# Performance work log

Hardware: AMD Instinct MI355X
Metric: run time of the kernel (lower is better)

Reference implementation:

```python
import jax, jax.numpy as jnp
import numpy as np

DIM = 512

def setup_inputs() -> dict:
    key = jax.random.key(0)
    kx, kq, kk, kv = jax.random.split(key, 4)
    x = jax.random.normal(kx, (8, 2048, DIM), dtype=jnp.float32)
    # Dense kernels are [in_dim, out_dim], no bias
    Wq = jax.random.normal(kq, (DIM, DIM), dtype=jnp.float32) * (DIM ** -0.5)
    Wk = jax.random.normal(kk, (DIM, DIM), dtype=jnp.float32) * (DIM ** -0.5)
    Wv = jax.random.normal(kv, (DIM, DIM), dtype=jnp.float32) * (DIM ** -0.5)
    return {"x": x, "Wq": Wq, "Wk": Wk, "Wv": Wv}

def reference(x, Wq, Wk, Wv):
    # x: [b, s, d]
    q = jnp.einsum('bsd,de->bse', x, Wq)
    k = jnp.einsum('bsd,de->bse', x, Wk)
    v = jnp.einsum('bsd,de->bse', x, Wv)
    scale = jnp.sqrt(jnp.asarray(DIM, dtype=x.dtype))
    attn = jnp.einsum('bqe,bke->bqk', q, k) / scale  # [b, s, s]
    attn = jax.nn.softmax(attn, axis=-1)
    return jnp.einsum('bqk,bke->bqe', attn, v)  # [b, s, d]
```

## Files before the change

kernel.cpp:

```cpp
#include <hip/hip_runtime.h>
#include <stdint.h>

typedef unsigned short u16;
typedef unsigned int u32;
typedef float floatx4 __attribute__((ext_vector_type(4)));
typedef __bf16 bf16x8 __attribute__((ext_vector_type(8)));
typedef __attribute__((address_space(1))) const u32 gu32;
typedef __attribute__((address_space(3))) u32 lu32;

#define SEQ 2048
#define DIM 512
#define NBATCH 8
#define TOTS (NBATCH * SEQ)

#if defined(__has_builtin)
#if __has_builtin(__builtin_amdgcn_cvt_pk_bf16_f32)
#define HAVE_PK_BF16 1
#endif
#endif
#ifndef HAVE_PK_BF16
#define HAVE_PK_BF16 0
#endif

__device__ __forceinline__ u16 f2bf(float f) {
#if HAVE_PK_BF16
  auto p = __builtin_amdgcn_cvt_pk_bf16_f32(f, f);
  union { decltype(p) v; u16 u[2]; } cv; cv.v = p;
  return cv.u[0];
#else
  u32 u = __float_as_uint(f);
  u += 0x7fffu + ((u >> 16) & 1u);
  return (u16)(u >> 16);
#endif
}


__device__ __forceinline__ void stageA(const u16* __restrict__ g, int ld, int k0, u16* lds) {
  const int t = threadIdx.x;
  const int wave = t >> 6, lane = t & 63;
  const int rsub = lane >> 3;
  const int lg = (lane & 7) ^ rsub;
#pragma unroll
  for (int q = 0; q < 4; ++q) {
    const int chunk = wave * 4 + q;
    const int row = chunk * 8 + rsub;
    const u16* gp = g + (size_t)row * ld + k0 + lg * 8;
    u16* lp = lds + chunk * 512 + lane * 8;
    __builtin_amdgcn_global_load_lds((gu32*)gp, (lu32*)lp, 16, 0, 0);
  }
}

__device__ __forceinline__ void stageB(const u16* __restrict__ g, int ld, int k0, u16* lds) {
  const int t = threadIdx.x;
  const int wave = t >> 6, lane = t & 63;
  const int rsub = lane >> 3;
  const int lg = (lane & 7) ^ rsub;
#pragma unroll
  for (int q = 0; q < 2; ++q) {
    const int chunk = wave * 2 + q;
    const int row = chunk * 8 + rsub;
    const u16* gp = g + (size_t)row * ld + k0 + lg * 8;
    u16* lp = lds + chunk * 512 + lane * 8;
    __builtin_amdgcn_global_load_lds((gu32*)gp, (lu32*)lp, 16, 0, 0);
  }
}

__device__ __forceinline__ void gemm_ring(const u16* __restrict__ A, int lda,
                                          const u16* __restrict__ BT, int ldb, int kdim,
                                          u16* As, u16* Bs, floatx4 acc[4][4]) {
  const int t = threadIdx.x;
  const int w = t >> 6, lane = t & 63;
  const int wm = w & 3, wn = w >> 2;
  const int l15 = lane & 15, quad = lane >> 4;
  const int swz = l15 & 7;
  const int nsteps = kdim >> 6;

  stageA(A, lda, 0, As);           stageB(BT, ldb, 0, Bs);
  stageA(A, lda, 64, As + 16384);  stageB(BT, ldb, 64, Bs + 8192);

  int slot = 0;
  for (int kt = 0; kt < nsteps; ++kt) {
    if (kt + 1 < nsteps) asm volatile("s_waitcnt vmcnt(6)" ::: "memory");
    else                 asm volatile("s_waitcnt vmcnt(0)" ::: "memory");
    __builtin_amdgcn_s_barrier();
    asm volatile("" ::: "memory");
    if (kt + 2 < nsteps) {
      int ss = slot + 2; if (ss >= 3) ss -= 3;
      stageA(A, lda, (kt + 2) << 6, As + ss * 16384);
      stageB(BT, ldb, (kt + 2) << 6, Bs + ss * 8192);
    }
    const u16* Ac = As + slot * 16384;
    const u16* Bc = Bs + slot * 8192;
#pragma unroll
    for (int ks = 0; ks < 2; ++ks) {
      const int pg = ((ks << 2) + quad) ^ swz;
      bf16x8 af[4], bfr[4];
#pragma unroll
      for (int i = 0; i < 4; ++i) {
        af[i]  = *(const bf16x8*)(Ac + (wm * 64 + i * 16 + l15) * 64 + pg * 8);
        bfr[i] = *(const bf16x8*)(Bc + (wn * 64 + i * 16 + l15) * 64 + pg * 8);
      }
#pragma unroll
      for (int mi = 0; mi < 4; ++mi)
#pragma unroll
        for (int ni = 0; ni < 4; ++ni)
          acc[mi][ni] = __builtin_amdgcn_mfma_f32_16x16x32_bf16(af[mi], bfr[ni], acc[mi][ni], 0, 0, 0);
    }
    ++slot; if (slot == 3) slot = 0;
  }
}

__device__ __forceinline__ void zero_acc(floatx4 acc[4][4]) {
#pragma unroll
  for (int i = 0; i < 4; ++i)
#pragma unroll
    for (int j = 0; j < 4; ++j)
      acc[i][j] = (floatx4){0.f, 0.f, 0.f, 0.f};
}

__global__ __launch_bounds__(256) void k_prep(const float* __restrict__ x,
                                              const float* __restrict__ Wq, const float* __restrict__ Wk,
                                              const float* __restrict__ Wv,
                                              u16* __restrict__ xb, u16* __restrict__ wt) {
  __shared__ float tile[64][65];
  const int t = threadIdx.x;
  if (blockIdx.x < 4096) {
    size_t i = ((size_t)blockIdx.x * 256 + t) * 8;
    float4 a = *(const float4*)(x + i);
    float4 b = *(const float4*)(x + i + 4);
    u16 o[8] = {f2bf(a.x), f2bf(a.y), f2bf(a.z), f2bf(a.w),
                f2bf(b.x), f2bf(b.y), f2bf(b.z), f2bf(b.w)};
    *(uint4*)(xb + i) = *(const uint4*)o;
    return;
  }
  const int r = blockIdx.x - 4096;
  const int sec = r >> 6, rem = r & 63;
  const int kb = (rem & 7) * 64, nb0 = (rem >> 3) * 64;
  const float* W = (sec == 0) ? Wq : (sec == 1) ? Wk : Wv;
#pragma unroll
  for (int i = 0; i < 4; ++i) {
    int kr = i * 16 + (t >> 4), nc = (t & 15) * 4;
    float4 v = *(const float4*)&W[(size_t)(kb + kr) * 512 + nb0 + nc];
    tile[kr][nc] = v.x; tile[kr][nc + 1] = v.y; tile[kr][nc + 2] = v.z; tile[kr][nc + 3] = v.w;
  }
  __syncthreads();
#pragma unroll
  for (int i = 0; i < 4; ++i) {
    int nr = i * 16 + (t >> 4), kc = (t & 15) * 4;
    u16 o[4] = {f2bf(tile[kc][nr]), f2bf(tile[kc + 1][nr]), f2bf(tile[kc + 2][nr]), f2bf(tile[kc + 3][nr])};
    *(uint2*)&wt[(size_t)(sec * 512 + nb0 + nr) * 512 + kb + kc] = *(const uint2*)o;
  }
}

__global__ __launch_bounds__(512, 2) void k_proj(const u16* __restrict__ xb, const u16* __restrict__ wt,
                                                 u16* __restrict__ qo, u16* __restrict__ ko,
                                                 u16* __restrict__ vt) {
  __shared__ __align__(16) u16 As[3 * 256 * 64];
  __shared__ __align__(16) u16 Bs[3 * 128 * 64];
  const int gx = blockIdx.x;
  floatx4 acc[4][4];
  zero_acc(acc);
  const int t = threadIdx.x, w = t >> 6, lane = t & 63;
  const int wm = w & 3, wn = w >> 2;
  const int l15 = lane & 15, quad = lane >> 4;
  if (gx < 512) {
    const int m0 = (gx & 63) * 256, n0 = (gx >> 6) * 128;
    gemm_ring(xb + (size_t)m0 * DIM, DIM, wt + (size_t)n0 * DIM, DIM, DIM, As, Bs, acc);
    const int sec = n0 >> 9;
    u16* __restrict__ C = sec ? ko : qo;
    const float scl = sec ? 1.0f : 0.04419417382415922f;
#pragma unroll
    for (int mi = 0; mi < 4; ++mi)
#pragma unroll
      for (int ni = 0; ni < 4; ++ni)
#pragma unroll
        for (int r = 0; r < 4; ++r) {
          int m = m0 + wm * 64 + mi * 16 + quad * 4 + r;
          int nc = (n0 + wn * 64 + ni * 16 + l15) & 511;
          C[(size_t)m * DIM + nc] = f2bf(acc[mi][ni][r] * scl);
        }
  } else {
    const int rr = gx - 512;
    const int m0 = (rr & 1) * 256;
    const int n0 = (rr >> 1) * 128;
    gemm_ring(wt + (size_t)(2 * DIM + m0) * DIM, DIM, xb + (size_t)n0 * DIM, DIM, DIM, As, Bs, acc);
#pragma unroll
    for (int mi = 0; mi < 4; ++mi)
#pragma unroll
      for (int ni = 0; ni < 4; ++ni)
#pragma unroll
        for (int r = 0; r < 4; ++r) {
          int m = m0 + wm * 64 + mi * 16 + quad * 4 + r;
          int n = n0 + wn * 64 + ni * 16 + l15;
          vt[(size_t)m * TOTS + n] = f2bf(acc[mi][ni][r]);
        }
  }
}

__global__ __launch_bounds__(512, 2) void k_scores(const u16* __restrict__ q, const u16* __restrict__ kk,
                                                   u16* __restrict__ sc, float* __restrict__ rowsum,
                                                   int b0) {
  __shared__ __align__(16) u16 As[3 * 256 * 64];
  __shared__ __align__(16) u16 Bs[3 * 128 * 64];
  const int bz = blockIdx.z, bb = b0 + bz;
  const int xcd = blockIdx.x & 7, j = blockIdx.x >> 3;
  const int n0 = (xcd * 2 + (j & 1)) * 128;
  const int m0 = (j >> 1) * 256;
  floatx4 acc[4][4];
  zero_acc(acc);
  gemm_ring(q + (size_t)bb * SEQ * DIM + (size_t)m0 * DIM, DIM,
            kk + (size_t)bb * SEQ * DIM + (size_t)n0 * DIM, DIM, DIM, As, Bs, acc);
  u16* C = sc + (size_t)bz * SEQ * SEQ;
  float* rsb = rowsum + (size_t)bb * SEQ;
  const int t = threadIdx.x, w = t >> 6, lane = t & 63;
  const int wm = w & 3, wn = w >> 2;
  const int l15 = lane & 15, quad = lane >> 4;
#pragma unroll
  for (int mi = 0; mi < 4; ++mi)
#pragma unroll
    for (int r = 0; r < 4; ++r) {
      int m = m0 + wm * 64 + mi * 16 + quad * 4 + r;
      float p = 0.f;
      float ev[4];
#pragma unroll
      for (int ni = 0; ni < 4; ++ni) {
        ev[ni] = __expf(acc[mi][ni][r]);
        p += ev[ni];
      }
#pragma unroll
      for (int ni = 0; ni < 4; ++ni) {
        int n = n0 + wn * 64 + ni * 16 + l15;
        C[(size_t)m * SEQ + n] = f2bf(ev[ni]);
      }
      p += __shfl_xor(p, 1); p += __shfl_xor(p, 2);
      p += __shfl_xor(p, 4); p += __shfl_xor(p, 8);
      if (l15 == 0) atomicAdd(&rsb[m], p);
    }
}

__global__ __launch_bounds__(512, 2) void k_pv(const u16* __restrict__ sc, const u16* __restrict__ vt,
                                               const float* __restrict__ rowsum,
                                               float* __restrict__ out, int b0) {
  __shared__ __align__(16) u16 As[3 * 256 * 64];
  __shared__ __align__(16) u16 Bs[3 * 128 * 64];
  const int bz = blockIdx.z, bb = b0 + bz;
  const int xcd = blockIdx.x & 7, j = blockIdx.x >> 3;
  const int m0 = xcd * 256, n0 = j * 128;
  floatx4 acc[4][4];
  zero_acc(acc);
  gemm_ring(sc + (size_t)bz * SEQ * SEQ + (size_t)m0 * SEQ, SEQ,
            vt + (size_t)n0 * TOTS + (size_t)bb * SEQ, TOTS, SEQ, As, Bs, acc);
  float* C = out + (size_t)bb * SEQ * DIM;
  const float* rsb = rowsum + (size_t)bb * SEQ;
  const int t = threadIdx.x, w = t >> 6, lane = t & 63;
  const int wm = w & 3, wn = w >> 2;
  const int l15 = lane & 15, quad = lane >> 4;
#pragma unroll
  for (int mi = 0; mi < 4; ++mi)
#pragma unroll
    for (int r = 0; r < 4; ++r) {
      int m = m0 + wm * 64 + mi * 16 + quad * 4 + r;
      float inv = 1.0f / rsb[m];
#pragma unroll
      for (int ni = 0; ni < 4; ++ni) {
        int n = n0 + wn * 64 + ni * 16 + l15;
        C[(size_t)m * DIM + n] = acc[mi][ni][r] * inv;
      }
    }
}

extern "C" void kernel_launch(void* const* d_in, const int* in_sizes, int n_in,
                              void* d_out, int out_size, void* d_ws, size_t ws_size,
                              hipStream_t stream) {
  const float* x  = (const float*)d_in[0];
  const float* Wq = (const float*)d_in[1];
  const float* Wk = (const float*)d_in[2];
  const float* Wv = (const float*)d_in[3];
  float* out = (float*)d_out;
  char* ws = (char*)d_ws;

  u16* xb   = (u16*)(ws + 0);
  u16* wt   = (u16*)(ws + 16777216);
  u16* qo   = (u16*)(ws + 18350080);
  u16* ko   = (u16*)(ws + 35127296);
  u16* vt   = (u16*)(ws + 51904512);
  float* rs = (float*)(ws + 68681728);
  u16* sc   = (u16*)(ws + 68747264);
  const size_t base_need = 68747264;
  const size_t per_b = (size_t)SEQ * SEQ * 2;
  size_t avail = (ws_size > base_need) ? (ws_size - base_need) : 0;
  int nb = (int)(avail / per_b);
  if (nb < 1) nb = 1;
  if (nb > NBATCH) nb = NBATCH;

  hipMemsetAsync(rs, 0, (size_t)NBATCH * SEQ * sizeof(float), stream);
  k_prep<<<dim3(4288), dim3(256), 0, stream>>>(x, Wq, Wk, Wv, xb, wt);
  k_proj<<<dim3(768), dim3(512), 0, stream>>>(xb, wt, qo, ko, vt);
  for (int b0 = 0; b0 < NBATCH; b0 += nb) {
    int nbr = (NBATCH - b0 < nb) ? (NBATCH - b0) : nb;
    k_scores<<<dim3(128, 1, nbr), dim3(512), 0, stream>>>(qo, ko, sc, rs, b0);
    k_pv<<<dim3(32, 1, nbr), dim3(512), 0, stream>>>(sc, vt, rs, out, b0);
  }
}
```

Baseline: 234.1 us.

## Interleave global-to-LDS prefetch with MFMA sub-steps using ping-pong barriers and setprio

```diff
diff --git a/kernel.cpp b/kernel.cpp
--- a/kernel.cpp
+++ b/kernel.cpp
@@ -34,14 +34,21 @@
 #endif
 }
 
-
-__device__ __forceinline__ void stageA(const u16* __restrict__ g, int ld, int k0, u16* lds) {
+__device__ __forceinline__ void barrier_f() {
+  asm volatile("" ::: "memory");
+  __builtin_amdgcn_s_barrier();
+  asm volatile("" ::: "memory");
+}
+
+
+template<int PART>
+__device__ __forceinline__ void stageA_h(const u16* __restrict__ g, int ld, int k0, u16* lds) {
   const int t = threadIdx.x;
   const int wave = t >> 6, lane = t & 63;
   const int rsub = lane >> 3;
   const int lg = (lane & 7) ^ rsub;
 #pragma unroll
-  for (int q = 0; q < 4; ++q) {
+  for (int q = PART * 2; q < PART * 2 + 2; ++q) {
     const int chunk = wave * 4 + q;
     const int row = chunk * 8 + rsub;
     const u16* gp = g + (size_t)row * ld + k0 + lg * 8;
@@ -50,19 +57,24 @@
   }
 }
 
-__device__ __forceinline__ void stageB(const u16* __restrict__ g, int ld, int k0, u16* lds) {
+template<int PART>
+__device__ __forceinline__ void stageB_h(const u16* __restrict__ g, int ld, int k0, u16* lds) {
   const int t = threadIdx.x;
   const int wave = t >> 6, lane = t & 63;
   const int rsub = lane >> 3;
   const int lg = (lane & 7) ^ rsub;
-#pragma unroll
-  for (int q = 0; q < 2; ++q) {
-    const int chunk = wave * 2 + q;
-    const int row = chunk * 8 + rsub;
-    const u16* gp = g + (size_t)row * ld + k0 + lg * 8;
-    u16* lp = lds + chunk * 512 + lane * 8;
-    __builtin_amdgcn_global_load_lds((gu32*)gp, (lu32*)lp, 16, 0, 0);
-  }
+  const int chunk = wave * 2 + PART;
+  const int row = chunk * 8 + rsub;
+  const u16* gp = g + (size_t)row * ld + k0 + lg * 8;
+  u16* lp = lds + chunk * 512 + lane * 8;
+  __builtin_amdgcn_global_load_lds((gu32*)gp, (lu32*)lp, 16, 0, 0);
+}
+
+__device__ __forceinline__ void stageA(const u16* __restrict__ g, int ld, int k0, u16* lds) {
+  stageA_h<0>(g, ld, k0, lds); stageA_h<1>(g, ld, k0, lds);
+}
+__device__ __forceinline__ void stageB(const u16* __restrict__ g, int ld, int k0, u16* lds) {
+  stageB_h<0>(g, ld, k0, lds); stageB_h<1>(g, ld, k0, lds);
 }
 
 __device__ __forceinline__ void gemm_ring(const u16* __restrict__ A, int lda,
@@ -77,20 +89,16 @@
 
   stageA(A, lda, 0, As);           stageB(BT, ldb, 0, Bs);
   stageA(A, lda, 64, As + 16384);  stageB(BT, ldb, 64, Bs + 8192);
+  asm volatile("s_waitcnt vmcnt(6)" ::: "memory");
+  barrier_f();
 
   int slot = 0;
   for (int kt = 0; kt < nsteps; ++kt) {
-    if (kt + 1 < nsteps) asm volatile("s_waitcnt vmcnt(6)" ::: "memory");
-    else                 asm volatile("s_waitcnt vmcnt(0)" ::: "memory");
-    __builtin_amdgcn_s_barrier();
-    asm volatile("" ::: "memory");
-    if (kt + 2 < nsteps) {
-      int ss = slot + 2; if (ss >= 3) ss -= 3;
-      stageA(A, lda, (kt + 2) << 6, As + ss * 16384);
-      stageB(BT, ldb, (kt + 2) << 6, Bs + ss * 8192);
-    }
     const u16* Ac = As + slot * 16384;
     const u16* Bc = Bs + slot * 8192;
+    int ss = slot + 2; if (ss >= 3) ss -= 3;
+    const bool st = (kt + 2 < nsteps);
+    const int k2 = (kt + 2) << 6;
 #pragma unroll
     for (int ks = 0; ks < 2; ++ks) {
       const int pg = ((ks << 2) + quad) ^ swz;
@@ -100,11 +108,26 @@
         af[i]  = *(const bf16x8*)(Ac + (wm * 64 + i * 16 + l15) * 64 + pg * 8);
         bfr[i] = *(const bf16x8*)(Bc + (wn * 64 + i * 16 + l15) * 64 + pg * 8);
       }
+      if (st) {
+        if (ks == 0) { stageA_h<0>(A, lda, k2, As + ss * 16384); stageB_h<0>(BT, ldb, k2, Bs + ss * 8192); }
+        else         { stageA_h<1>(A, lda, k2, As + ss * 16384); stageB_h<1>(BT, ldb, k2, Bs + ss * 8192); }
+      }
+      barrier_f();
+      asm volatile("s_waitcnt lgkmcnt(0)" ::: "memory");
+      __builtin_amdgcn_sched_barrier(0);
+      __builtin_amdgcn_s_setprio(1);
 #pragma unroll
       for (int mi = 0; mi < 4; ++mi)
 #pragma unroll
         for (int ni = 0; ni < 4; ++ni)
           acc[mi][ni] = __builtin_amdgcn_mfma_f32_16x16x32_bf16(af[mi], bfr[ni], acc[mi][ni], 0, 0, 0);
+      __builtin_amdgcn_s_setprio(0);
+      __builtin_amdgcn_sched_barrier(0);
+      if (ks == 1) {
+        if (kt + 2 < nsteps)      asm volatile("s_waitcnt vmcnt(6)" ::: "memory");
+        else if (kt + 1 < nsteps) asm volatile("s_waitcnt vmcnt(0)" ::: "memory");
+      }
+      barrier_f();
     }
     ++slot; if (slot == 3) slot = 0;
   }
```

Measured after the change: 224.1 us. 1.04x faster.

## Enlarge GEMM tiles to 256x256 with double-buffered LDS and fold rowsum zeroing

Applied to the files above, without the earlier changes.

```diff
diff --git a/kernel.cpp b/kernel.cpp
--- a/kernel.cpp
+++ b/kernel.cpp
@@ -34,15 +34,22 @@
 #endif
 }
 
-
-__device__ __forceinline__ void stageA(const u16* __restrict__ g, int ld, int k0, u16* lds) {
+__device__ __forceinline__ void barrier_f() {
+  asm volatile("" ::: "memory");
+  __builtin_amdgcn_s_barrier();
+  asm volatile("" ::: "memory");
+}
+
+
+template<int NL>
+__device__ __forceinline__ void stage_t(const u16* __restrict__ g, int ld, int k0, u16* lds) {
   const int t = threadIdx.x;
   const int wave = t >> 6, lane = t & 63;
   const int rsub = lane >> 3;
   const int lg = (lane & 7) ^ rsub;
 #pragma unroll
-  for (int q = 0; q < 4; ++q) {
-    const int chunk = wave * 4 + q;
+  for (int q = 0; q < NL; ++q) {
+    const int chunk = wave * NL + q;
     const int row = chunk * 8 + rsub;
     const u16* gp = g + (size_t)row * ld + k0 + lg * 8;
     u16* lp = lds + chunk * 512 + lane * 8;
@@ -50,69 +57,67 @@
   }
 }
 
-__device__ __forceinline__ void stageB(const u16* __restrict__ g, int ld, int k0, u16* lds) {
-  const int t = threadIdx.x;
-  const int wave = t >> 6, lane = t & 63;
-  const int rsub = lane >> 3;
-  const int lg = (lane & 7) ^ rsub;
-#pragma unroll
-  for (int q = 0; q < 2; ++q) {
-    const int chunk = wave * 2 + q;
-    const int row = chunk * 8 + rsub;
-    const u16* gp = g + (size_t)row * ld + k0 + lg * 8;
-    u16* lp = lds + chunk * 512 + lane * 8;
-    __builtin_amdgcn_global_load_lds((gu32*)gp, (lu32*)lp, 16, 0, 0);
-  }
-}
-
-__device__ __forceinline__ void gemm_ring(const u16* __restrict__ A, int lda,
-                                          const u16* __restrict__ BT, int ldb, int kdim,
-                                          u16* As, u16* Bs, floatx4 acc[4][4]) {
+template<int MREP>
+__device__ __forceinline__ void gemm_big(const u16* __restrict__ A, int lda,
+                                         const u16* __restrict__ BT, int ldb, int kdim,
+                                         u16* As, u16* Bs, floatx4 acc[][4]) {
+  constexpr int ASLOT = MREP * 128 * 64;
+  constexpr int BSLOT = 256 * 64;
   const int t = threadIdx.x;
   const int w = t >> 6, lane = t & 63;
-  const int wm = w & 3, wn = w >> 2;
+  const int wm = w >> 2, wn = w & 3;
   const int l15 = lane & 15, quad = lane >> 4;
   const int swz = l15 & 7;
   const int nsteps = kdim >> 6;
 
-  stageA(A, lda, 0, As);           stageB(BT, ldb, 0, Bs);
-  stageA(A, lda, 64, As + 16384);  stageB(BT, ldb, 64, Bs + 8192);
-
-  int slot = 0;
+  stage_t<2 * MREP>(A, lda, 0, As);
+  stage_t<4>(BT, ldb, 0, Bs);
+
   for (int kt = 0; kt < nsteps; ++kt) {
-    if (kt + 1 < nsteps) asm volatile("s_waitcnt vmcnt(6)" ::: "memory");
-    else                 asm volatile("s_waitcnt vmcnt(0)" ::: "memory");
-    __builtin_amdgcn_s_barrier();
-    asm volatile("" ::: "memory");
-    if (kt + 2 < nsteps) {
-      int ss = slot + 2; if (ss >= 3) ss -= 3;
-      stageA(A, lda, (kt + 2) << 6, As + ss * 16384);
-      stageB(BT, ldb, (kt + 2) << 6, Bs + ss * 8192);
+    const u16* Ac = As + (kt & 1) * ASLOT;
+    const u16* Bc = Bs + (kt & 1) * BSLOT;
+    if (kt + 1 < nsteps) {
+      stage_t<2 * MREP>(A, lda, (kt + 1) << 6, As + ((kt + 1) & 1) * ASLOT);
+      stage_t<4>(BT, ldb, (kt + 1) << 6, Bs + ((kt + 1) & 1) * BSLOT);
+      if constexpr (MREP == 2) asm volatile("s_waitcnt vmcnt(8)" ::: "memory");
+      else                     asm volatile("s_waitcnt vmcnt(6)" ::: "memory");
+    } else {
+      asm volatile("s_waitcnt vmcnt(0)" ::: "memory");
     }
-    const u16* Ac = As + slot * 16384;
-    const u16* Bc = Bs + slot * 8192;
-#pragma unroll
-    for (int ks = 0; ks < 2; ++ks) {
-      const int pg = ((ks << 2) + quad) ^ swz;
-      bf16x8 af[4], bfr[4];
-#pragma unroll
-      for (int i = 0; i < 4; ++i) {
-        af[i]  = *(const bf16x8*)(Ac + (wm * 64 + i * 16 + l15) * 64 + pg * 8);
-        bfr[i] = *(const bf16x8*)(Bc + (wn * 64 + i * 16 + l15) * 64 + pg * 8);
-      }
+    barrier_f();
+
+    bf16x8 bfr[4];
+#pragma unroll
+    for (int p = 0; p < 2 * MREP; ++p) {
+      const int ksl = (MREP == 2) ? (p >> 1) : p;
+      const int mh  = (MREP == 2) ? (p & 1) : 0;
+      const int pg = ((ksl << 2) + quad) ^ swz;
+      if (mh == 0) {
+#pragma unroll
+        for (int i = 0; i < 4; ++i)
+          bfr[i] = *(const bf16x8*)(Bc + (wn * 64 + i * 16 + l15) * 64 + pg * 8);
+      }
+      bf16x8 af[4];
+#pragma unroll
+      for (int i = 0; i < 4; ++i)
+        af[i] = *(const bf16x8*)(Ac + (wm * MREP * 64 + mh * 64 + i * 16 + l15) * 64 + pg * 8);
+      __builtin_amdgcn_s_setprio(1);
 #pragma unroll
       for (int mi = 0; mi < 4; ++mi)
 #pragma unroll
         for (int ni = 0; ni < 4; ++ni)
-          acc[mi][ni] = __builtin_amdgcn_mfma_f32_16x16x32_bf16(af[mi], bfr[ni], acc[mi][ni], 0, 0, 0);
+          acc[mh * 4 + mi][ni] =
+              __builtin_amdgcn_mfma_f32_16x16x32_bf16(af[mi], bfr[ni], acc[mh * 4 + mi][ni], 0, 0, 0);
+      __builtin_amdgcn_s_setprio(0);
     }
-    ++slot; if (slot == 3) slot = 0;
-  }
-}
-
-__device__ __forceinline__ void zero_acc(floatx4 acc[4][4]) {
-#pragma unroll
-  for (int i = 0; i < 4; ++i)
+    barrier_f();
+  }
+}
+
+template<int NACC>
+__device__ __forceinline__ void zero_acc(floatx4 acc[][4]) {
+#pragma unroll
+  for (int i = 0; i < NACC; ++i)
 #pragma unroll
     for (int j = 0; j < 4; ++j)
       acc[i][j] = (floatx4){0.f, 0.f, 0.f, 0.f};
@@ -154,77 +159,82 @@
 
 __global__ __launch_bounds__(512, 2) void k_proj(const u16* __restrict__ xb, const u16* __restrict__ wt,
                                                  u16* __restrict__ qo, u16* __restrict__ ko,
-                                                 u16* __restrict__ vt) {
-  __shared__ __align__(16) u16 As[3 * 256 * 64];
-  __shared__ __align__(16) u16 Bs[3 * 128 * 64];
+                                                 u16* __restrict__ vt, float* __restrict__ rs) {
+  __shared__ __align__(16) u16 As[2 * 256 * 64];
+  __shared__ __align__(16) u16 Bs[2 * 256 * 64];
   const int gx = blockIdx.x;
-  floatx4 acc[4][4];
-  zero_acc(acc);
+  if (gx < 16) {
+    float4 z = {0.f, 0.f, 0.f, 0.f};
+    float* p = rs + ((size_t)gx * 512 + threadIdx.x) * 8;
+    *(float4*)p = z; *(float4*)(p + 4) = z;
+  }
+  floatx4 acc[8][4];
+  zero_acc<8>(acc);
   const int t = threadIdx.x, w = t >> 6, lane = t & 63;
-  const int wm = w & 3, wn = w >> 2;
+  const int wm = w >> 2, wn = w & 3;
   const int l15 = lane & 15, quad = lane >> 4;
-  if (gx < 512) {
-    const int m0 = (gx & 63) * 256, n0 = (gx >> 6) * 128;
-    gemm_ring(xb + (size_t)m0 * DIM, DIM, wt + (size_t)n0 * DIM, DIM, DIM, As, Bs, acc);
+  if (gx < 256) {
+    const int m0 = (gx & 63) * 256, n0 = (gx >> 6) * 256;
+    gemm_big<2>(xb + (size_t)m0 * DIM, DIM, wt + (size_t)n0 * DIM, DIM, DIM, As, Bs, acc);
     const int sec = n0 >> 9;
     u16* __restrict__ C = sec ? ko : qo;
     const float scl = sec ? 1.0f : 0.04419417382415922f;
 #pragma unroll
-    for (int mi = 0; mi < 4; ++mi)
-#pragma unroll
-      for (int ni = 0; ni < 4; ++ni)
-#pragma unroll
-        for (int r = 0; r < 4; ++r) {
-          int m = m0 + wm * 64 + mi * 16 + quad * 4 + r;
+    for (int a = 0; a < 8; ++a)
+#pragma unroll
+      for (int r = 0; r < 4; ++r) {
+        int m = m0 + wm * 128 + (a >> 2) * 64 + (a & 3) * 16 + quad * 4 + r;
+#pragma unroll
+        for (int ni = 0; ni < 4; ++ni) {
           int nc = (n0 + wn * 64 + ni * 16 + l15) & 511;
-          C[(size_t)m * DIM + nc] = f2bf(acc[mi][ni][r] * scl);
+          C[(size_t)m * DIM + nc] = f2bf(acc[a][ni][r] * scl);
         }
+      }
   } else {
-    const int rr = gx - 512;
+    const int rr = gx - 256;
     const int m0 = (rr & 1) * 256;
-    const int n0 = (rr >> 1) * 128;
-    gemm_ring(wt + (size_t)(2 * DIM + m0) * DIM, DIM, xb + (size_t)n0 * DIM, DIM, DIM, As, Bs, acc);
-#pragma unroll
-    for (int mi = 0; mi < 4; ++mi)
-#pragma unroll
-      for (int ni = 0; ni < 4; ++ni)
-#pragma unroll
-        for (int r = 0; r < 4; ++r) {
-          int m = m0 + wm * 64 + mi * 16 + quad * 4 + r;
+    const int n0 = (rr >> 1) * 256;
+    gemm_big<2>(wt + (size_t)(2 * DIM + m0) * DIM, DIM, xb + (size_t)n0 * DIM, DIM, DIM, As, Bs, acc);
+#pragma unroll
+    for (int a = 0; a < 8; ++a)
+#pragma unroll
+      for (int r = 0; r < 4; ++r) {
+        int m = m0 + wm * 128 + (a >> 2) * 64 + (a & 3) * 16 + quad * 4 + r;
+#pragma unroll
+        for (int ni = 0; ni < 4; ++ni) {
           int n = n0 + wn * 64 + ni * 16 + l15;
-          vt[(size_t)m * TOTS + n] = f2bf(acc[mi][ni][r]);
+          vt[(size_t)m * TOTS + n] = f2bf(acc[a][ni][r]);
         }
+      }
   }
 }
 
 __global__ __launch_bounds__(512, 2) void k_scores(const u16* __restrict__ q, const u16* __restrict__ kk,
                                                    u16* __restrict__ sc, float* __restrict__ rowsum,
                                                    int b0) {
-  __shared__ __align__(16) u16 As[3 * 256 * 64];
-  __shared__ __align__(16) u16 Bs[3 * 128 * 64];
+  __shared__ __align__(16) u16 As[2 * 256 * 64];
+  __shared__ __align__(16) u16 Bs[2 * 256 * 64];
   const int bz = blockIdx.z, bb = b0 + bz;
-  const int xcd = blockIdx.x & 7, j = blockIdx.x >> 3;
-  const int n0 = (xcd * 2 + (j & 1)) * 128;
-  const int m0 = (j >> 1) * 256;
-  floatx4 acc[4][4];
-  zero_acc(acc);
-  gemm_ring(q + (size_t)bb * SEQ * DIM + (size_t)m0 * DIM, DIM,
-            kk + (size_t)bb * SEQ * DIM + (size_t)n0 * DIM, DIM, DIM, As, Bs, acc);
+  const int m0 = (blockIdx.x >> 3) * 256, n0 = (blockIdx.x & 7) * 256;
+  floatx4 acc[8][4];
+  zero_acc<8>(acc);
+  gemm_big<2>(q + (size_t)bb * SEQ * DIM + (size_t)m0 * DIM, DIM,
+              kk + (size_t)bb * SEQ * DIM + (size_t)n0 * DIM, DIM, DIM, As, Bs, acc);
   u16* C = sc + (size_t)bz * SEQ * SEQ;
   float* rsb = rowsum + (size_t)bb * SEQ;
   const int t = threadIdx.x, w = t >> 6, lane = t & 63;
-  const int wm = w & 3, wn = w >> 2;
+  const int wm = w >> 2, wn = w & 3;
   const int l15 = lane & 15, quad = lane >> 4;
 #pragma unroll
-  for (int mi = 0; mi < 4; ++mi)
+  for (int a = 0; a < 8; ++a)
 #pragma unroll
     for (int r = 0; r < 4; ++r) {
-      int m = m0 + wm * 64 + mi * 16 + quad * 4 + r;
+      int m = m0 + wm * 128 + (a >> 2) * 64 + (a & 3) * 16 + quad * 4 + r;
       float p = 0.f;
       float ev[4];
 #pragma unroll
       for (int ni = 0; ni < 4; ++ni) {
-        ev[ni] = __expf(acc[mi][ni][r]);
+        ev[ni] = __expf(acc[a][ni][r]);
         p += ev[ni];
       }
 #pragma unroll
@@ -241,30 +251,29 @@
 __global__ __launch_bounds__(512, 2) void k_pv(const u16* __restrict__ sc, const u16* __restrict__ vt,
                                                const float* __restrict__ rowsum,
                                                float* __restrict__ out, int b0) {
-  __shared__ __align__(16) u16 As[3 * 256 * 64];
-  __shared__ __align__(16) u16 Bs[3 * 128 * 64];
+  __shared__ __align__(16) u16 As[2 * 128 * 64];
+  __shared__ __align__(16) u16 Bs[2 * 256 * 64];
   const int bz = blockIdx.z, bb = b0 + bz;
-  const int xcd = blockIdx.x & 7, j = blockIdx.x >> 3;
-  const int m0 = xcd * 256, n0 = j * 128;
+  const int m0 = (blockIdx.x >> 1) * 128, n0 = (blockIdx.x & 1) * 256;
   floatx4 acc[4][4];
-  zero_acc(acc);
-  gemm_ring(sc + (size_t)bz * SEQ * SEQ + (size_t)m0 * SEQ, SEQ,
-            vt + (size_t)n0 * TOTS + (size_t)bb * SEQ, TOTS, SEQ, As, Bs, acc);
+  zero_acc<4>(acc);
+  gemm_big<1>(sc + (size_t)bz * SEQ * SEQ + (size_t)m0 * SEQ, SEQ,
+              vt + (size_t)n0 * TOTS + (size_t)bb * SEQ, TOTS, SEQ, As, Bs, acc);
   float* C = out + (size_t)bb * SEQ * DIM;
   const float* rsb = rowsum + (size_t)bb * SEQ;
   const int t = threadIdx.x, w = t >> 6, lane = t & 63;
-  const int wm = w & 3, wn = w >> 2;
+  const int wm = w >> 2, wn = w & 3;
   const int l15 = lane & 15, quad = lane >> 4;
 #pragma unroll
-  for (int mi = 0; mi < 4; ++mi)
+  for (int a = 0; a < 4; ++a)
 #pragma unroll
     for (int r = 0; r < 4; ++r) {
-      int m = m0 + wm * 64 + mi * 16 + quad * 4 + r;
+      int m = m0 + wm * 64 + a * 16 + quad * 4 + r;
       float inv = 1.0f / rsb[m];
 #pragma unroll
       for (int ni = 0; ni < 4; ++ni) {
         int n = n0 + wn * 64 + ni * 16 + l15;
-        C[(size_t)m * DIM + n] = acc[mi][ni][r] * inv;
+        C[(size_t)m * DIM + n] = acc[a][ni][r] * inv;
       }
     }
 }
@@ -293,12 +302,11 @@
   if (nb < 1) nb = 1;
   if (nb > NBATCH) nb = NBATCH;
 
-  hipMemsetAsync(rs, 0, (size_t)NBATCH * SEQ * sizeof(float), stream);
   k_prep<<<dim3(4288), dim3(256), 0, stream>>>(x, Wq, Wk, Wv, xb, wt);
-  k_proj<<<dim3(768), dim3(512), 0, stream>>>(xb, wt, qo, ko, vt);
+  k_proj<<<dim3(384), dim3(512), 0, stream>>>(xb, wt, qo, ko, vt, rs);
   for (int b0 = 0; b0 < NBATCH; b0 += nb) {
     int nbr = (NBATCH - b0 < nb) ? (NBATCH - b0) : nb;
-    k_scores<<<dim3(128, 1, nbr), dim3(512), 0, stream>>>(qo, ko, sc, rs, b0);
+    k_scores<<<dim3(64, 1, nbr), dim3(512), 0, stream>>>(qo, ko, sc, rs, b0);
     k_pv<<<dim3(32, 1, nbr), dim3(512), 0, stream>>>(sc, vt, rs, out, b0);
   }
 }
```

Result: faster. 224.6 us (-4.1%).
